# Kernel optimization log

Measured on AMD Instinct MI355X. Metric: run time of the kernel, lower is better.

## Reference

```python
import jax, jax.numpy as jnp
import numpy as np
import math

NEG_INF = -1e9
B, S, P, HID, NH, DH = 2, 1024, 128, 1024, 16, 64
NUM_SEG = 2


def setup_inputs() -> dict:
    key = jax.random.key(0)
    ks = jax.random.split(key, 16)
    f32 = jnp.float32
    inp = {
        'content_stream': jax.random.normal(ks[0], (B, S, HID), f32),
        'query_stream': jax.random.normal(ks[1], (B, P, HID), f32),
        'positional_encoding': jax.random.normal(ks[2], (B, 2 * S, HID), f32),
        'segment_matrix': jax.random.randint(ks[3], (B, S, S), 0, 2) > 0,
        'segment_encoding': jax.random.normal(ks[4], (NUM_SEG, NH, DH), f32) * 0.02,
        'segment_bias': jax.random.normal(ks[5], (NH, DH), f32) * 0.02,
        'content_mask': (jax.random.uniform(ks[6], (B, 1, S, S)) < 0.1).astype(f32),
        'query_mask': (jax.random.uniform(ks[7], (B, 1, S, S)) < 0.1).astype(f32),
        'target_mapping': jax.nn.one_hot(jax.random.randint(ks[8], (B, P), 0, S), S, dtype=f32),
        'content_bias': jax.random.normal(ks[9], (NH, DH), f32) * 0.02,
        'position_bias': jax.random.normal(ks[10], (NH, DH), f32) * 0.02,
        # projection params (no bias, XLNet-style split/merge projections)
        'wq': jax.random.normal(ks[11], (HID, NH, DH), f32) * 0.02,
        'wkc': jax.random.normal(ks[12], (HID, NH, DH), f32) * 0.02,
        'wv': jax.random.normal(ks[13], (HID, NH, DH), f32) * 0.02,
        'wkp': jax.random.normal(ks[14], (HID, NH, DH), f32) * 0.02,
        'wo': jax.random.normal(ks[15], (NH, DH, HID), f32) * 0.02,
    }
    return inp


def _rel_shift(x, klen):
    # x: [B, H, Q, R]; TransformerXL pad/reshape/slice relative shift, then keep cols 1:1+klen
    b, h, q, r = x.shape
    padded = jnp.pad(x, ((0, 0), (0, 0), (0, 0), (1, 0)))
    shifted = padded.reshape(b, h, r + 1, q)[:, :, 1:].reshape(b, h, q, r)
    return shifted[..., 1:1 + klen]


def _attention(q, kc, v, kp, content_bias, position_bias,
               segment_matrix, segment_encoding, segment_bias, token_mask):
    # q,kc,v: [B,S,H,D]; kp: [B,2S,H,D]
    content = jnp.einsum('bqhd,brhd->bhqr', q + content_bias, kc)          # [B,H,S,S]
    position = jnp.einsum('bqhd,brhd->bhqr', q + position_bias, kp)        # [B,H,S,2S]
    position = _rel_shift(position, content.shape[-1])                     # [B,H,S,S]
    segment = jnp.einsum('bqhd,shd->bhqs', q + segment_bias, segment_encoding)  # [B,H,S,2]
    segment = jnp.where(segment_matrix[:, None], segment[..., 1:], segment[..., :1])  # [B,H,S,S]
    scores = (content + position + segment) * (1.0 / math.sqrt(DH))
    scores = scores + token_mask * NEG_INF
    weights = jax.nn.softmax(scores, axis=-1)  # dropout is identity at inference
    return jnp.einsum('bhqr,brhd->bqhd', weights, v)


def reference(content_stream, query_stream, positional_encoding, segment_matrix,
              segment_encoding, segment_bias, content_mask, query_mask,
              target_mapping, content_bias, position_bias,
              wq, wkc, wv, wkp, wo):
    split = lambda x, w: jnp.einsum('bth,hnd->btnd', x, w)
    # state is None -> keys/values come from content_stream only
    q = split(content_stream, wq)
    kc = split(content_stream, wkc)
    v = split(content_stream, wv)
    kp = split(positional_encoding, wkp)

    content_out = _attention(q, kc, v, kp, content_bias, position_bias,
                             segment_matrix, segment_encoding, segment_bias, content_mask)
    content_output = jnp.einsum('bqnd,ndh->bqh', content_out, wo)

    qg = split(query_stream, wq)                                   # [B,P,H,D]
    qg = jnp.einsum('bphd,bpq->bqhd', qg, target_mapping)          # scatter to [B,S,H,D]
    query_out = _attention(qg, kc, v, kp, content_bias, position_bias,
                           segment_matrix, segment_encoding, segment_bias, query_mask)
    query_out = jnp.einsum('bqhd,bpq->bphd', query_out, target_mapping)  # gather back to [B,P,H,D]
    query_output = jnp.einsum('bpnd,ndh->bph', query_out, wo)

    return content_output, query_output
```

## Files before the change

kernel.cpp:

```cpp
#include <hip/hip_runtime.h>
#include <math.h>


#define NEG_INF_F (-1e9f)

static constexpr int Bc  = 2;
static constexpr int Sc  = 1024;
static constexpr int Pc  = 128;
static constexpr int HIDc = 1024;
static constexpr int NHc = 16;
static constexpr int DHc = 64;

typedef __bf16 bf16;
typedef __bf16 bf16x8 __attribute__((ext_vector_type(8)));
typedef float  f32x4  __attribute__((ext_vector_type(4)));

#define MFMA16(a, b, c) __builtin_amdgcn_mfma_f32_16x16x32_bf16((a), (b), (c), 0, 0, 0)

__global__ void sniff_seg(const unsigned char* __restrict__ seg, int* __restrict__ flag) {
    const int t = threadIdx.x;
    int nz1 = 0, nz23 = 0;
    for (int i = t * 64; i < t * 64 + 64; ++i) {
        unsigned char c = seg[i];
        int m = i & 3;
        if (m == 1 && c) nz1 = 1;
        if ((m == 2 || m == 3) && c) nz23 = 1;
    }
    nz1 = __any(nz1);
    nz23 = __any(nz23);
    if (t == 0) flag[0] = nz1 ? 0 : (nz23 ? 2 : 1);
}

__global__ void bits3(const void* __restrict__ seg, const int* __restrict__ flag,
                      const float* __restrict__ cm, const float* __restrict__ qm,
                      unsigned* __restrict__ segb, unsigned* __restrict__ cmb,
                      unsigned* __restrict__ qmb) {
    const int bid = blockIdx.x;
    const int which = bid >> 8;
    const int idx = (bid & 255) * 256 + threadIdx.x;
    unsigned wv = 0;
    if (which == 0) {
        const int mode = flag[0];
        if (mode == 0) {
            const unsigned char* s = (const unsigned char*)seg + (size_t)idx * 32;
#pragma unroll
            for (int k = 0; k < 32; ++k) wv |= (s[k] != 0) ? (1u << k) : 0u;
        } else if (mode == 1) {
            const int* s = (const int*)seg + (size_t)idx * 32;
#pragma unroll
            for (int k = 0; k < 32; ++k) wv |= (s[k] != 0) ? (1u << k) : 0u;
        } else {
            const float* s = (const float*)seg + (size_t)idx * 32;
#pragma unroll
            for (int k = 0; k < 32; ++k) wv |= (s[k] != 0.f) ? (1u << k) : 0u;
        }
        segb[idx] = wv;
    } else {
        const float* s = (which == 1 ? cm : qm) + (size_t)idx * 32;
#pragma unroll
        for (int k = 0; k < 32; ++k) wv |= (s[k] != 0.f) ? (1u << k) : 0u;
        (which == 1 ? cmb : qmb)[idx] = wv;
    }
}

__global__ __launch_bounds__(256) void prep_split(
        const float* __restrict__ content, const float* __restrict__ posenc,
        const float* __restrict__ querys,
        const float* __restrict__ wq, const float* __restrict__ wkc,
        const float* __restrict__ wvp, const float* __restrict__ wkp,
        const float* __restrict__ wo,
        bf16* __restrict__ ch, bf16* __restrict__ cl,
        bf16* __restrict__ ph, bf16* __restrict__ pl,
        bf16* __restrict__ qh, bf16* __restrict__ ql,
        bf16* __restrict__ wqkvh, bf16* __restrict__ wqkvl,
        bf16* __restrict__ wkphh, bf16* __restrict__ wkpll,
        bf16* __restrict__ woh, bf16* __restrict__ wol) {
    __shared__ float tile[32][33];
    const int bid = blockIdx.x;
    if (bid < 3200) {
        const float* src; bf16 *hdst, *ldst; size_t base;
        if (bid < 1024)      { src = content; hdst = ch; ldst = cl; base = (size_t)bid * 2048; }
        else if (bid < 3072) { src = posenc;  hdst = ph; ldst = pl; base = (size_t)(bid - 1024) * 2048; }
        else                 { src = querys;  hdst = qh; ldst = ql; base = (size_t)(bid - 3072) * 2048; }
        const size_t i = base + (size_t)threadIdx.x * 8;
        float xs[8];
        *(float4*)xs       = *(const float4*)(src + i);
        *(float4*)(xs + 4) = *(const float4*)(src + i + 4);
        union { bf16 b[8]; uint4 u; } H, L;
#pragma unroll
        for (int k = 0; k < 8; ++k) {
            bf16 hb = (bf16)xs[k];
            H.b[k] = hb;
            L.b[k] = (bf16)(xs[k] - (float)hb);
        }
        *(uint4*)(hdst + i) = H.u;
        *(uint4*)(ldst + i) = L.u;
        return;
    }
    const int wid = bid - 3200;
    const int z = wid >> 10, rem = wid & 1023;
    const float* W = z == 0 ? wq : z == 1 ? wkc : z == 2 ? wvp : z == 3 ? wkp : wo;
    bf16* Th = z < 3 ? wqkvh + (size_t)z * HIDc * HIDc : (z == 3 ? wkphh : woh);
    bf16* Tl = z < 3 ? wqkvl + (size_t)z * HIDc * HIDc : (z == 3 ? wkpll : wol);
    const int k0 = (rem >> 5) * 32, n0 = (rem & 31) * 32;
    const int c = threadIdx.x & 31, r0 = threadIdx.x >> 5;
#pragma unroll
    for (int rr = 0; rr < 4; ++rr) {
        int r = r0 + rr * 8;
        tile[r][c] = W[(size_t)(k0 + r) * HIDc + n0 + c];
    }
    __syncthreads();
#pragma unroll
    for (int rr = 0; rr < 4; ++rr) {
        int n = r0 + rr * 8;
        float x = tile[c][n];
        bf16 hb = (bf16)x;
        Th[(size_t)(n0 + n) * HIDc + k0 + c] = hb;
        Tl[(size_t)(n0 + n) * HIDc + k0 + c] = (bf16)(x - (float)hb);
    }
}

__global__ __launch_bounds__(256) void big_gemm(
        const bf16* __restrict__ conth, const bf16* __restrict__ contl,
        const bf16* __restrict__ posh, const bf16* __restrict__ posl,
        const bf16* __restrict__ quh, const bf16* __restrict__ qul,
        const bf16* __restrict__ wqkvh, const bf16* __restrict__ wqkvl,
        const bf16* __restrict__ wkph, const bf16* __restrict__ wkpl,
        float* __restrict__ qf, bf16* __restrict__ kch,
        bf16* __restrict__ vtg, bf16* __restrict__ kpho,
        float* __restrict__ qgf) {
    __shared__ bf16 AhS[128][40], AlS[128][40], BhS[128][40], BlS[128][40];
    const int bid = blockIdx.x;
    const int vb = (bid & 7) * 82 + (bid >> 3);
    int mode, bx, by;
    const bf16 *Ahp, *Alp, *Bhp, *Blp;
    if (vb < 384)      { mode = 1; bx = vb >> 4; by = vb & 15;
                          Ahp = conth; Alp = contl; Bhp = wqkvh; Blp = wqkvl; }
    else if (vb < 640) { mode = 2; int r = vb - 384; bx = r >> 5; by = r & 31;
                          Ahp = posh;  Alp = posl;  Bhp = wkph;  Blp = wkpl; }
    else               { mode = 0; int r = vb - 640; bx = r & 7; by = r >> 3;
                          Ahp = quh;   Alp = qul;   Bhp = wqkvh; Blp = wqkvl; }
    const int t = threadIdx.x, lane = t & 63, wv = t >> 6;
    const int g = lane >> 4, ml = lane & 15;
    const int m0 = by * 128, n0 = bx * 128;
    const int moff = (wv & 1) * 64, noff = (wv >> 1) * 64;
    const int row2 = t >> 1, c16 = (t & 1) * 16;
    const int K = HIDc;

    f32x4 acc[4][4];
#pragma unroll
    for (int i = 0; i < 4; ++i)
#pragma unroll
        for (int j = 0; j < 4; ++j) acc[i][j] = (f32x4){0.f, 0.f, 0.f, 0.f};

    uint4 rah0, rah1, ral0, ral1, rbh0, rbh1, rbl0, rbl1;
    auto gload = [&](int k0) {
        size_t ab = (size_t)(m0 + row2) * K + k0 + c16;
        rah0 = *(const uint4*)(Ahp + ab);
        rah1 = *(const uint4*)(Ahp + ab + 8);
        ral0 = *(const uint4*)(Alp + ab);
        ral1 = *(const uint4*)(Alp + ab + 8);
        size_t bb = (size_t)(n0 + row2) * K + k0 + c16;
        rbh0 = *(const uint4*)(Bhp + bb);
        rbh1 = *(const uint4*)(Bhp + bb + 8);
        rbl0 = *(const uint4*)(Blp + bb);
        rbl1 = *(const uint4*)(Blp + bb + 8);
    };
    gload(0);

    for (int k0 = 0; k0 < K; k0 += 32) {
        __syncthreads();
        *(uint4*)&AhS[row2][c16]     = rah0;
        *(uint4*)&AhS[row2][c16 + 8] = rah1;
        *(uint4*)&AlS[row2][c16]     = ral0;
        *(uint4*)&AlS[row2][c16 + 8] = ral1;
        *(uint4*)&BhS[row2][c16]     = rbh0;
        *(uint4*)&BhS[row2][c16 + 8] = rbh1;
        *(uint4*)&BlS[row2][c16]     = rbl0;
        *(uint4*)&BlS[row2][c16 + 8] = rbl1;
        __syncthreads();
        if (k0 + 32 < K) gload(k0 + 32);
        bf16x8 afh[4], afl[4], bfh[4], bfl[4];
#pragma unroll
        for (int i = 0; i < 4; ++i) {
            afh[i] = *(const bf16x8*)&AhS[moff + i * 16 + ml][g * 8];
            afl[i] = *(const bf16x8*)&AlS[moff + i * 16 + ml][g * 8];
            bfh[i] = *(const bf16x8*)&BhS[noff + i * 16 + ml][g * 8];
            bfl[i] = *(const bf16x8*)&BlS[noff + i * 16 + ml][g * 8];
        }
#pragma unroll
        for (int i = 0; i < 4; ++i)
#pragma unroll
            for (int j = 0; j < 4; ++j) {
                acc[i][j] = MFMA16(afl[i], bfh[j], acc[i][j]);
                acc[i][j] = MFMA16(afh[i], bfl[j], acc[i][j]);
                acc[i][j] = MFMA16(afh[i], bfh[j], acc[i][j]);
            }
    }
#pragma unroll
    for (int j = 0; j < 4; ++j) {
        const int nb = n0 + noff + j * 16;
#pragma unroll
        for (int i = 0; i < 4; ++i) {
            const int mbase = m0 + moff + i * 16 + g * 4;
            if (mode == 0) {
#pragma unroll
                for (int r = 0; r < 4; ++r)
                    qgf[(size_t)(mbase + r) * 1024 + nb + ml] = acc[i][j][r];
            } else if (mode == 2) {
                int hh = nb >> 6, d = (nb & 63) + ml;
#pragma unroll
                for (int r = 0; r < 4; ++r) {
                    int m = mbase + r, b = m >> 11, s = m & 2047;
                    kpho[((size_t)(b * 16 + hh) * 2048 + s) * 64 + d] = (bf16)acc[i][j][r];
                }
            } else {
                int reg = nb >> 10, nc = nb & 1023;
                if (reg == 0) {
#pragma unroll
                    for (int r = 0; r < 4; ++r)
                        qf[(size_t)(mbase + r) * 1024 + nc + ml] = acc[i][j][r];
                } else if (reg == 1) {
                    int hh = nc >> 6, d = (nc & 63) + ml;
#pragma unroll
                    for (int r = 0; r < 4; ++r) {
                        int m = mbase + r, b = m >> 10, s = m & 1023;
                        kch[((size_t)(b * 16 + hh) * 1024 + s) * 64 + d] = (bf16)acc[i][j][r];
                    }
                } else {
                    int hh = nc >> 6, d = (nc & 63) + ml;
                    int b = mbase >> 10, sb_ = mbase & 1023;
                    union { bf16 v[4]; uint2 u; } pk;
#pragma unroll
                    for (int r = 0; r < 4; ++r) pk.v[r] = (bf16)acc[i][j][r];
                    *(uint2*)(vtg + ((size_t)(b * 16 + hh) * 64 + d) * 1024 + sb_) = pk.u;
                }
            }
        }
    }
}

__global__ __launch_bounds__(256) void gemm_wo64(
        const bf16* __restrict__ a1h, const bf16* __restrict__ a1l,
        const bf16* __restrict__ a2h, const bf16* __restrict__ a2l,
        const bf16* __restrict__ Bhp, const bf16* __restrict__ Blp,
        float* __restrict__ out1, float* __restrict__ out2) {
    __shared__ bf16 AhS[64][40], AlS[64][40], BhS[128][40], BlS[128][40];
    const int bid = blockIdx.x;
    const int vb = (bid & 7) * 36 + (bid >> 3);
    const bf16 *Ahp, *Alp; float* Cf; int m0, n0;
    if (vb < 256) { Ahp = a1h; Alp = a1l; Cf = out1; m0 = (vb & 31) * 64; n0 = (vb >> 5) * 128; }
    else          { int r = vb - 256; Ahp = a2h; Alp = a2l; Cf = out2;
                    m0 = (r & 3) * 64; n0 = (r >> 2) * 128; }
    const int t = threadIdx.x, lane = t & 63, wv = t >> 6;
    const int g = lane >> 4, ml = lane & 15;
    const int moff = (wv & 1) * 32, noff = (wv >> 1) * 64;
    const int arow = t >> 2, ac8 = (t & 3) * 8;
    const int brow = t >> 1, bc16 = (t & 1) * 16;
    const int K = HIDc, N = HIDc;

    f32x4 acc[2][4];
#pragma unroll
    for (int i = 0; i < 2; ++i)
#pragma unroll
        for (int j = 0; j < 4; ++j) acc[i][j] = (f32x4){0.f, 0.f, 0.f, 0.f};

    uint4 rah, ral, rbh0, rbh1, rbl0, rbl1;
    auto gload = [&](int k0) {
        size_t ao = (size_t)(m0 + arow) * K + k0 + ac8;
        rah = *(const uint4*)(Ahp + ao);
        ral = *(const uint4*)(Alp + ao);
        size_t bo = (size_t)(n0 + brow) * K + k0 + bc16;
        rbh0 = *(const uint4*)(Bhp + bo);
        rbh1 = *(const uint4*)(Bhp + bo + 8);
        rbl0 = *(const uint4*)(Blp + bo);
        rbl1 = *(const uint4*)(Blp + bo + 8);
    };
    gload(0);

    for (int k0 = 0; k0 < K; k0 += 32) {
        __syncthreads();
        *(uint4*)&AhS[arow][ac8]      = rah;
        *(uint4*)&AlS[arow][ac8]      = ral;
        *(uint4*)&BhS[brow][bc16]     = rbh0;
        *(uint4*)&BhS[brow][bc16 + 8] = rbh1;
        *(uint4*)&BlS[brow][bc16]     = rbl0;
        *(uint4*)&BlS[brow][bc16 + 8] = rbl1;
        __syncthreads();
        if (k0 + 32 < K) gload(k0 + 32);
        bf16x8 afh[2], afl[2], bfh[4], bfl[4];
#pragma unroll
        for (int i = 0; i < 2; ++i) {
            afh[i] = *(const bf16x8*)&AhS[moff + i * 16 + ml][g * 8];
            afl[i] = *(const bf16x8*)&AlS[moff + i * 16 + ml][g * 8];
        }
#pragma unroll
        for (int j = 0; j < 4; ++j) {
            bfh[j] = *(const bf16x8*)&BhS[noff + j * 16 + ml][g * 8];
            bfl[j] = *(const bf16x8*)&BlS[noff + j * 16 + ml][g * 8];
        }
#pragma unroll
        for (int i = 0; i < 2; ++i)
#pragma unroll
            for (int j = 0; j < 4; ++j) {
                acc[i][j] = MFMA16(afl[i], bfh[j], acc[i][j]);
                acc[i][j] = MFMA16(afh[i], bfl[j], acc[i][j]);
                acc[i][j] = MFMA16(afh[i], bfh[j], acc[i][j]);
            }
    }
#pragma unroll
    for (int i = 0; i < 2; ++i)
#pragma unroll
        for (int j = 0; j < 4; ++j)
#pragma unroll
            for (int r = 0; r < 4; ++r)
                Cf[(size_t)(m0 + moff + i * 16 + g * 4 + r) * N + n0 + noff + j * 16 + ml] =
                    acc[i][j][r];
}

__global__ void find_idx(const float* __restrict__ tm, int* __restrict__ idxb,
                         float* __restrict__ wgtb) {
    const int bp = blockIdx.x;
    const float* row = tm + (size_t)bp * Sc;
    __shared__ int sidx;
    if (threadIdx.x == 0) sidx = 0;
    __syncthreads();
    for (int j = threadIdx.x; j < Sc; j += 256)
        if (row[j] != 0.f) atomicMax(&sidx, j);
    __syncthreads();
    if (threadIdx.x == 0) { idxb[bp] = sidx; wgtb[bp] = row[sidx]; }
}

__global__ void scatter_add(const int* __restrict__ idxb, const float* __restrict__ wgtb,
                            const float* __restrict__ qgf, float* __restrict__ qsf) {
    const int bp = blockIdx.x;
    const int b = bp >> 7;
    const int q = idxb[bp];
    const float w = wgtb[bp];
    const int e = threadIdx.x * 4;
    float4 v = *(const float4*)(qgf + (size_t)bp * HIDc + e);
    float* dst = qsf + ((size_t)(b * Sc) + q) * HIDc + e;
    atomicAdd(dst + 0, w * v.x);
    atomicAdd(dst + 1, w * v.y);
    atomicAdd(dst + 2, w * v.z);
    atomicAdd(dst + 3, w * v.w);
}

__global__ void gather_o(const int* __restrict__ idxb, const float* __restrict__ wgtb,
                         const bf16* __restrict__ ah, const bf16* __restrict__ al,
                         bf16* __restrict__ gh, bf16* __restrict__ gl) {
    const int bp = blockIdx.x;
    const int b = bp >> 7;
    const int q = idxb[bp];
    const float w = wgtb[bp];
    const int e = threadIdx.x * 4;
    const size_t so = ((size_t)(b * Sc) + q) * HIDc + e;
#pragma unroll
    for (int k = 0; k < 4; ++k) {
        float v = ((float)ah[so + k] + (float)al[so + k]) * w;
        bf16 hb = (bf16)v;
        gh[(size_t)bp * HIDc + e + k] = hb;
        gl[(size_t)bp * HIDc + e + k] = (bf16)(v - (float)hb);
    }
}

__global__ __launch_bounds__(256, 4) void attn_fused(
        const float* __restrict__ qcf, const float* __restrict__ qqf,
        const bf16* __restrict__ kch, const bf16* __restrict__ vtg,
        const bf16* __restrict__ kph,
        const float* __restrict__ cb, const float* __restrict__ pb,
        const float* __restrict__ sb, const float* __restrict__ senc,
        const unsigned* __restrict__ sbits,
        const unsigned* __restrict__ cmb, const unsigned* __restrict__ qmb,
        bf16* __restrict__ aoh1, bf16* __restrict__ aol1,
        bf16* __restrict__ aoh2, bf16* __restrict__ aol2) {
    __shared__ bf16 kcS[32][72];
    __shared__ bf16 kpS[96][72];
    __shared__ float Rw[4][16][48];
    __shared__ bf16 Pw[4][16][40];

    const int bid = blockIdx.x;
    const int vb = (bid & 7) * 128 + (bid >> 3);
    const int qb = vb & 15, strm = (vb >> 4) & 1, h = (vb >> 5) & 15, b = vb >> 9;
    const int q0 = qb * 64;

    const float* qf = strm ? qqf : qcf;
    const unsigned* mbits = strm ? qmb : cmb;
    bf16* aoh = strm ? aoh2 : aoh1;
    bf16* aol = strm ? aol2 : aol1;

    const int t = threadIdx.x, w = t >> 6, lane = t & 63, g = lane >> 4, ml = lane & 15;

    const int qrow = q0 + w * 16 + ml;
    const float* qrp = qf + (size_t)(b * Sc + qrow) * HIDc + h * DHc;
    float qe[16], cbe[16], pbe[16], sbe[16], e0e[16], e1e[16];
    {
        const float* cbp = cb + h * DHc;
        const float* pbp = pb + h * DHc;
        const float* sbp = sb + h * DHc;
        const float* e0p = senc + h * DHc;
        const float* e1p = senc + NHc * DHc + h * DHc;
#pragma unroll
        for (int kk = 0; kk < 2; ++kk) {
            int o = kk * 32 + g * 8;
            *(float4*)(qe + kk * 8)      = *(const float4*)(qrp + o);
            *(float4*)(qe + kk * 8 + 4)  = *(const float4*)(qrp + o + 4);
            *(float4*)(cbe + kk * 8)     = *(const float4*)(cbp + o);
            *(float4*)(cbe + kk * 8 + 4) = *(const float4*)(cbp + o + 4);
            *(float4*)(pbe + kk * 8)     = *(const float4*)(pbp + o);
            *(float4*)(pbe + kk * 8 + 4) = *(const float4*)(pbp + o + 4);
            *(float4*)(sbe + kk * 8)     = *(const float4*)(sbp + o);
            *(float4*)(sbe + kk * 8 + 4) = *(const float4*)(sbp + o + 4);
            *(float4*)(e0e + kk * 8)     = *(const float4*)(e0p + o);
            *(float4*)(e0e + kk * 8 + 4) = *(const float4*)(e0p + o + 4);
            *(float4*)(e1e + kk * 8)     = *(const float4*)(e1p + o);
            *(float4*)(e1e + kk * 8 + 4) = *(const float4*)(e1p + o + 4);
        }
    }
    bf16x8 qch[2], qcl[2], qph[2], qpl[2];
    float s0 = 0.f, s1 = 0.f;
#pragma unroll
    for (int kk = 0; kk < 2; ++kk) {
#pragma unroll
        for (int i = 0; i < 8; ++i) {
            float qv = qe[kk * 8 + i];
            float xc = qv + cbe[kk * 8 + i];
            float xp = qv + pbe[kk * 8 + i];
            bf16 hb = (bf16)xc;
            qch[kk][i] = hb; qcl[kk][i] = (bf16)(xc - (float)hb);
            hb = (bf16)xp;
            qph[kk][i] = hb; qpl[kk][i] = (bf16)(xp - (float)hb);
            float qs = qv + sbe[kk * 8 + i];
            s0 += qs * e0e[kk * 8 + i];
            s1 += qs * e1e[kk * 8 + i];
        }
    }
    s0 += __shfl_xor(s0, 16); s0 += __shfl_xor(s0, 32);
    s1 += __shfl_xor(s1, 16); s1 += __shfl_xor(s1, 32);
    float d0v[4], d1v[4];
#pragma unroll
    for (int r = 0; r < 4; ++r) {
        d0v[r] = __shfl(s0, g * 4 + r);
        d1v[r] = __shfl(s1, g * 4 + r);
    }

    f32x4 oacc[4];
#pragma unroll
    for (int i = 0; i < 4; ++i) oacc[i] = (f32x4){0.f, 0.f, 0.f, 0.f};
    f32x4 lacc = (f32x4){0.f, 0.f, 0.f, 0.f};
    bf16x8 onesv;
#pragma unroll
    for (int i = 0; i < 8; ++i) onesv[i] = (bf16)1.0f;

    const size_t bh = (size_t)(b * 16 + h);
    const bf16* kcb = kch + bh * (Sc * DHc);
    const bf16* kpb = kph + bh * (2 * Sc * DHc);
    const bf16* vtb = vtg + bh * (DHc * Sc);
    const int woff = 48 - w * 16;
    const int base0 = Sc - q0 - 63;
    const size_t mrow0 = (size_t)(b * Sc + q0 + w * 16 + g * 4) * 32;

    const int tr = t >> 3, tc8 = (t & 7) * 8;

    const int wp0 = base0 % 96;
    {
        int g0 = base0 + tr;
        int g1 = base0 + 32 + tr;
        uint4 a0 = *(const uint4*)(kpb + (size_t)g0 * 64 + tc8);
        uint4 a1 = *(const uint4*)(kpb + (size_t)g1 * 64 + tc8);
        int p0 = wp0 + tr;      p0 -= (p0 >= 96) ? 96 : 0;
        int p1 = wp0 + 32 + tr; p1 -= (p1 >= 96) ? 96 : 0;
        p1 -= (p1 >= 96) ? 96 : 0;
        *(uint4*)&kpS[p0][tc8] = a0;
        *(uint4*)&kpS[p1][tc8] = a1;
    }
    uint4 pkc, pkp;
    {
        int gr = base0 + 64 + tr; gr = gr > 2 * Sc - 1 ? 2 * Sc - 1 : gr;
        pkp = *(const uint4*)(kpb + (size_t)gr * 64 + tc8);
        pkc = *(const uint4*)(kcb + (size_t)tr * 64 + tc8);
    }
    int wb = wp0 + 64; wb -= (wb >= 96) ? 96 : 0;
    int rb = wp0 + woff; rb -= (rb >= 96) ? 96 : 0;

    for (int j0 = 0; j0 < Sc; j0 += 32) {
        __syncthreads();
        {
            int pw = wb + tr; pw -= (pw >= 96) ? 96 : 0;
            *(uint4*)&kpS[pw][tc8] = pkp;
            *(uint4*)&kcS[tr][tc8] = pkc;
        }
        __syncthreads();
        {
            int nj = (j0 + 32 < Sc) ? j0 + 32 : j0;
            pkc = *(const uint4*)(kcb + (size_t)(nj + tr) * 64 + tc8);
            int gr = base0 + j0 + 96 + tr; gr = gr > 2 * Sc - 1 ? 2 * Sc - 1 : gr;
            pkp = *(const uint4*)(kpb + (size_t)gr * 64 + tc8);
        }
        wb += 32; wb -= (wb >= 96) ? 96 : 0;
        bf16x8 vfrag[4];
#pragma unroll
        for (int nt = 0; nt < 4; ++nt)
            vfrag[nt] = *(const bf16x8*)(vtb + (size_t)(nt * 16 + ml) * 1024 + j0 + g * 8);
        unsigned mw[4], sw_[4];
        const int wcol = j0 >> 5;
#pragma unroll
        for (int r = 0; r < 4; ++r) {
            mw[r]  = mbits[mrow0 + (size_t)r * 32 + wcol];
            sw_[r] = sbits[mrow0 + (size_t)r * 32 + wcol];
        }

        f32x4 accc[2];
#pragma unroll
        for (int jt = 0; jt < 2; ++jt) {
            f32x4 a = (f32x4){0.f, 0.f, 0.f, 0.f};
#pragma unroll
            for (int kk = 0; kk < 2; ++kk) {
                bf16x8 kf = *(const bf16x8*)&kcS[jt * 16 + ml][kk * 32 + g * 8];
                a = MFMA16(qcl[kk], kf, a);
                a = MFMA16(qch[kk], kf, a);
            }
            accc[jt] = a;
        }
#pragma unroll
        for (int ct = 0; ct < 3; ++ct) {
            int row = rb + ct * 16 + ml; row -= (row >= 96) ? 96 : 0;
            f32x4 a = (f32x4){0.f, 0.f, 0.f, 0.f};
#pragma unroll
            for (int kk = 0; kk < 2; ++kk) {
                bf16x8 kf = *(const bf16x8*)&kpS[row][kk * 32 + g * 8];
                a = MFMA16(qpl[kk], kf, a);
                a = MFMA16(qph[kk], kf, a);
            }
#pragma unroll
            for (int r = 0; r < 4; ++r) Rw[w][g * 4 + r][ct * 16 + ml] = a[r];
        }
        rb += 32; rb -= (rb >= 96) ? 96 : 0;

#pragma unroll
        for (int jt = 0; jt < 2; ++jt) {
            int jc = jt * 16 + ml;
#pragma unroll
            for (int r = 0; r < 4; ++r) {
                int row = g * 4 + r;
                float s = (accc[jt][r] + Rw[w][row][jc - row + 15] +
                           (((sw_[r] >> jc) & 1u) ? d1v[r] : d0v[r])) * 0.125f;
                if ((mw[r] >> jc) & 1u) s += NEG_INF_F;
                Pw[w][row][jc] = (bf16)__expf(s);
            }
        }
        bf16x8 pa = *(const bf16x8*)&Pw[w][ml][g * 8];
#pragma unroll
        for (int nt = 0; nt < 4; ++nt)
            oacc[nt] = MFMA16(pa, vfrag[nt], oacc[nt]);
        lacc = MFMA16(pa, onesv, lacc);
    }

    float inv[4];
#pragma unroll
    for (int r = 0; r < 4; ++r) inv[r] = 1.0f / lacc[r];
#pragma unroll
    for (int nt = 0; nt < 4; ++nt)
#pragma unroll
        for (int r = 0; r < 4; ++r) {
            float val = oacc[nt][r] * inv[r];
            size_t o = (size_t)(b * Sc + q0 + w * 16 + g * 4 + r) * HIDc + h * DHc + nt * 16 + ml;
            bf16 hb = (bf16)val;
            aoh[o] = hb;
            aol[o] = (bf16)(val - (float)hb);
        }
}

extern "C" void kernel_launch(void* const* d_in, const int* in_sizes, int n_in,
                              void* d_out, int out_size, void* d_ws, size_t ws_size,
                              hipStream_t stream) {
    const float* content = (const float*)d_in[0];
    const float* querys  = (const float*)d_in[1];
    const float* posenc  = (const float*)d_in[2];
    const void*  segraw  = d_in[3];
    const float* senc    = (const float*)d_in[4];
    const float* sbias   = (const float*)d_in[5];
    const float* cmask   = (const float*)d_in[6];
    const float* qmask   = (const float*)d_in[7];
    const float* tmap    = (const float*)d_in[8];
    const float* cbias   = (const float*)d_in[9];
    const float* pbias   = (const float*)d_in[10];
    const float* wq      = (const float*)d_in[11];
    const float* wkc     = (const float*)d_in[12];
    const float* wv      = (const float*)d_in[13];
    const float* wkp     = (const float*)d_in[14];
    const float* wo      = (const float*)d_in[15];
    float* out = (float*)d_out;

    char* ws = (char*)d_ws;
    size_t off = 0;
    auto take = [&](size_t bytes) -> char* {
        char* p = ws + off;
        off += (bytes + 255) & ~(size_t)255;
        return p;
    };
    int*      flag = (int*)take(256);
    int*      idxb = (int*)take(Bc * Pc * 4);
    float*    wgtb = (float*)take(Bc * Pc * 4);
    unsigned* segb = (unsigned*)take((size_t)Bc * Sc * 32 * 4);
    unsigned* cmb  = (unsigned*)take((size_t)Bc * Sc * 32 * 4);
    unsigned* qmb  = (unsigned*)take((size_t)Bc * Sc * 32 * 4);
    bf16* wqkvh = (bf16*)take((size_t)3 * HIDc * HIDc * 2);
    bf16* wqkvl = (bf16*)take((size_t)3 * HIDc * HIDc * 2);
    bf16* wkphw = (bf16*)take((size_t)HIDc * HIDc * 2);
    bf16* wkplw = (bf16*)take((size_t)HIDc * HIDc * 2);
    bf16* woh   = (bf16*)take((size_t)HIDc * HIDc * 2);
    bf16* wol   = (bf16*)take((size_t)HIDc * HIDc * 2);
    bf16* conth = (bf16*)take((size_t)Bc * Sc * HIDc * 2);
    bf16* contl = (bf16*)take((size_t)Bc * Sc * HIDc * 2);
    bf16* posh  = (bf16*)take((size_t)Bc * 2 * Sc * HIDc * 2);
    bf16* posl  = (bf16*)take((size_t)Bc * 2 * Sc * HIDc * 2);
    bf16* quh   = (bf16*)take((size_t)Bc * Pc * HIDc * 2);
    bf16* qul   = (bf16*)take((size_t)Bc * Pc * HIDc * 2);
    float* qf   = (float*)take((size_t)Bc * Sc * HIDc * 4);
    float* qsf  = (float*)take((size_t)Bc * Sc * HIDc * 4);
    bf16* kchp  = (bf16*)take((size_t)Bc * NHc * Sc * DHc * 2);
    bf16* kphp  = (bf16*)take((size_t)Bc * NHc * 2 * Sc * DHc * 2);
    bf16* vtg   = (bf16*)take((size_t)Bc * NHc * DHc * Sc * 2);
    float* qgf  = (float*)take((size_t)Bc * Pc * HIDc * 4);
    bf16* aoh1  = (bf16*)take((size_t)Bc * Sc * HIDc * 2);
    bf16* aol1  = (bf16*)take((size_t)Bc * Sc * HIDc * 2);
    bf16* aoh2  = (bf16*)take((size_t)Bc * Sc * HIDc * 2);
    bf16* aol2  = (bf16*)take((size_t)Bc * Sc * HIDc * 2);
    bf16* gathh = (bf16*)take((size_t)Bc * Pc * HIDc * 2);
    bf16* gathl = (bf16*)take((size_t)Bc * Pc * HIDc * 2);

    dim3 blk(256);

    sniff_seg<<<1, 64, 0, stream>>>((const unsigned char*)segraw, flag);
    bits3<<<768, blk, 0, stream>>>(segraw, flag, cmask, qmask, segb, cmb, qmb);
    find_idx<<<Bc * Pc, blk, 0, stream>>>(tmap, idxb, wgtb);
    prep_split<<<8320, blk, 0, stream>>>(content, posenc, querys,
                                         wq, wkc, wv, wkp, wo,
                                         conth, contl, posh, posl, quh, qul,
                                         wqkvh, wqkvl, wkphw, wkplw, woh, wol);

    big_gemm<<<656, blk, 0, stream>>>(conth, contl, posh, posl, quh, qul,
                                      wqkvh, wqkvl, wkphw, wkplw,
                                      qf, kchp, vtg, kphp, qgf);

    hipMemsetAsync(qsf, 0, (size_t)Bc * Sc * HIDc * 4, stream);
    scatter_add<<<Bc * Pc, blk, 0, stream>>>(idxb, wgtb, qgf, qsf);

    attn_fused<<<1024, blk, 0, stream>>>(qf, qsf, kchp, vtg, kphp,
                                         cbias, pbias, sbias, senc, segb, cmb, qmb,
                                         aoh1, aol1, aoh2, aol2);

    gather_o<<<Bc * Pc, blk, 0, stream>>>(idxb, wgtb, aoh2, aol2, gathh, gathl);
    gemm_wo64<<<288, blk, 0, stream>>>(aoh1, aol1, gathh, gathl, woh, wol,
                                       out, out + (size_t)Bc * Sc * HIDc);
}
```

Before: 271.5 us.

## Transpose score MFMA operands so each lane owns one query row

Swaps the A/B operands of the QK and QP MFMAs so each lane's accumulator holds four key columns for a single query row. This lets the mask and segment words be loaded once per lane rather than per row, removes the d0/d1 shuffles, and allows vectorised f32x4 stores to Rw and packed bf16 stores to Pw. Exponentials now use exp2f with a prescaled log2e factor, and masked entries are zeroed directly instead of adding a large negative value. The Rw row pitch is padded to 52 to reduce LDS bank conflicts on the transposed accesses, and the zeroed masks change numerics slightly.

```diff
diff --git a/kernel.cpp b/kernel.cpp
--- a/kernel.cpp
+++ b/kernel.cpp
@@ -1,8 +1,6 @@
 #include <hip/hip_runtime.h>
 #include <math.h>
 
-
-#define NEG_INF_F (-1e9f)
 
 static constexpr int Bc  = 2;
 static constexpr int Sc  = 1024;
@@ -376,7 +374,7 @@
         bf16* __restrict__ aoh2, bf16* __restrict__ aol2) {
     __shared__ bf16 kcS[32][72];
     __shared__ bf16 kpS[96][72];
-    __shared__ float Rw[4][16][48];
+    __shared__ float Rw[4][16][52];
     __shared__ bf16 Pw[4][16][40];
 
     const int bid = blockIdx.x;
@@ -437,12 +435,6 @@
     }
     s0 += __shfl_xor(s0, 16); s0 += __shfl_xor(s0, 32);
     s1 += __shfl_xor(s1, 16); s1 += __shfl_xor(s1, 32);
-    float d0v[4], d1v[4];
-#pragma unroll
-    for (int r = 0; r < 4; ++r) {
-        d0v[r] = __shfl(s0, g * 4 + r);
-        d1v[r] = __shfl(s1, g * 4 + r);
-    }
 
     f32x4 oacc[4];
 #pragma unroll
@@ -458,7 +450,8 @@
     const bf16* vtb = vtg + bh * (DHc * Sc);
     const int woff = 48 - w * 16;
     const int base0 = Sc - q0 - 63;
-    const size_t mrow0 = (size_t)(b * Sc + q0 + w * 16 + g * 4) * 32;
+    const size_t mrowq = (size_t)(b * Sc + qrow) * 32;
+    const float SCL2E = 0.125f * 1.44269504088896340736f;
 
     const int tr = t >> 3, tc8 = (t & 7) * 8;
 
@@ -502,13 +495,9 @@
 #pragma unroll
         for (int nt = 0; nt < 4; ++nt)
             vfrag[nt] = *(const bf16x8*)(vtb + (size_t)(nt * 16 + ml) * 1024 + j0 + g * 8);
-        unsigned mw[4], sw_[4];
         const int wcol = j0 >> 5;
-#pragma unroll
-        for (int r = 0; r < 4; ++r) {
-            mw[r]  = mbits[mrow0 + (size_t)r * 32 + wcol];
-            sw_[r] = sbits[mrow0 + (size_t)r * 32 + wcol];
-        }
+        const unsigned mw = mbits[mrowq + wcol];
+        const unsigned sw = sbits[mrowq + wcol];
 
         f32x4 accc[2];
 #pragma unroll
@@ -517,8 +506,8 @@
 #pragma unroll
             for (int kk = 0; kk < 2; ++kk) {
                 bf16x8 kf = *(const bf16x8*)&kcS[jt * 16 + ml][kk * 32 + g * 8];
-                a = MFMA16(qcl[kk], kf, a);
-                a = MFMA16(qch[kk], kf, a);
+                a = MFMA16(kf, qcl[kk], a);
+                a = MFMA16(kf, qch[kk], a);
             }
             accc[jt] = a;
         }
@@ -529,25 +518,26 @@
 #pragma unroll
             for (int kk = 0; kk < 2; ++kk) {
                 bf16x8 kf = *(const bf16x8*)&kpS[row][kk * 32 + g * 8];
-                a = MFMA16(qpl[kk], kf, a);
-                a = MFMA16(qph[kk], kf, a);
+                a = MFMA16(kf, qpl[kk], a);
+                a = MFMA16(kf, qph[kk], a);
             }
-#pragma unroll
-            for (int r = 0; r < 4; ++r) Rw[w][g * 4 + r][ct * 16 + ml] = a[r];
+            *(f32x4*)&Rw[w][ml][ct * 16 + g * 4] = a;
         }
         rb += 32; rb -= (rb >= 96) ? 96 : 0;
 
 #pragma unroll
         for (int jt = 0; jt < 2; ++jt) {
-            int jc = jt * 16 + ml;
+            union { bf16 v[4]; uint2 u; } pk;
 #pragma unroll
             for (int r = 0; r < 4; ++r) {
-                int row = g * 4 + r;
-                float s = (accc[jt][r] + Rw[w][row][jc - row + 15] +
-                           (((sw_[r] >> jc) & 1u) ? d1v[r] : d0v[r])) * 0.125f;
-                if ((mw[r] >> jc) & 1u) s += NEG_INF_F;
-                Pw[w][row][jc] = (bf16)__expf(s);
+                int jl = jt * 16 + g * 4 + r;
+                float s = (accc[jt][r] + Rw[w][ml][jl - ml + 15] +
+                           (((sw >> jl) & 1u) ? s1 : s0)) * SCL2E;
+                float p = exp2f(s);
+                p = ((mw >> jl) & 1u) ? 0.f : p;
+                pk.v[r] = (bf16)p;
             }
+            *(uint2*)&Pw[w][ml][jt * 16 + g * 4] = pk.u;
         }
         bf16x8 pa = *(const bf16x8*)&Pw[w][ml][g * 8];
 #pragma unroll
```

Result: faster. 264.3 us (-2.7%).
